# Kernel optimization log

Measured on AMD Instinct MI355X. Metric: run time of the kernel, lower is better.

Reference implementation:

```python
import jax, jax.numpy as jnp
import numpy as np

ALPHA = 0.2   # LeakyReLU slope
NEG = -9e15   # masked-attention fill, as in standard dense GAT


def _gat_multihead(h, edge_attr, adj, n2n, Wg, Weg, a_s, a_d, a_e, concat):
    # h: [N, I], edge_attr: [E, I], adj: [N, N], n2n: [N*N, I]
    # Wg, Weg: [H, I, O]; a_s, a_d, a_e: [H, O]
    H, I, O = Wg.shape
    N = h.shape[0]
    Wh = jnp.einsum('ni,hio->hno', h, Wg)                    # [H, N, O]
    es = jnp.einsum('hno,ho->hn', Wh, a_s)                   # [H, N] source logits
    ed = jnp.einsum('hno,ho->hn', Wh, a_d)                   # [H, N] dest logits
    ve = jnp.einsum('hio,ho->hi', Weg, a_e)                  # [H, I] fold edge proj into vector
    ee = (n2n @ ve.T).T.reshape(H, N, N)                     # [H, N, N] edge logits (row=src)
    e = jax.nn.leaky_relu(es[:, :, None] + ed[:, None, :] + ee, ALPHA)
    e = jnp.where(adj[None] > 0, e, NEG)
    attn = jax.nn.softmax(e, axis=-1)
    hout = jnp.einsum('hnm,hmo->nho', attn, Wh).reshape(N, H * O)
    eout = jnp.einsum('ei,hio->eho', edge_attr, Weg).reshape(-1, H * O)
    if concat:
        hout, eout = jax.nn.elu(hout), jax.nn.elu(eout)
    return hout, eout


def _edge_pool(x, edge_index, edge_attr, Wp, bp):
    # Deterministic static-shape variant of EdgePooling: merge node pairs (2k, 2k+1)
    # with a learned sigmoid score over the concatenated endpoint features.
    N, F = x.shape
    x2 = x.reshape(N // 2, 2, F)
    score = jax.nn.sigmoid(jnp.concatenate([x2[:, 0], x2[:, 1]], axis=1) @ Wp + bp)  # [N/2,1]
    new_x = (x2[:, 0] + x2[:, 1]) * score
    return new_x, edge_index // 2, edge_attr


def _global_attn(x, W, b):
    # GlobalAttention with gate_nn = Linear -> Sigmoid, softmax over the single graph
    gate = jax.nn.sigmoid(x @ W + b)          # [N, 1]
    alpha = jax.nn.softmax(gate, axis=0)
    return (alpha * x).sum(axis=0, keepdims=True)  # [1, F]


def _adj_n2n(N, edge_index, edge_attr):
    # Faithful vectorized version of _get_adj_node2node (scatter replaces python loop)
    src, dst = edge_index[0], edge_index[1]
    adj = jnp.zeros((N, N), edge_attr.dtype).at[src, dst].add(1.0)
    n2n = jnp.zeros((N * N, edge_attr.shape[1]), edge_attr.dtype).at[src * N + dst].set(edge_attr)
    return adj, n2n


def setup_inputs() -> dict:
    key = jax.random.key(0)
    ks = jax.random.split(key, 24)
    N, E, HID, NH = 512, 4096, 64, 16
    O = 2 * HID                                  # per-head GAT output = 128
    CAT = NH * O                                 # 2048
    s = 0.1
    features = jax.random.normal(ks[0], (N, HID), jnp.float32)
    edge_index = jax.random.randint(ks[1], (2, E), 0, N, jnp.int64)
    edge_attr = jax.random.normal(ks[2], (E, HID), jnp.float32)
    adjacency, n2n = _adj_n2n(N, edge_index, edge_attr)
    inp = dict(features=features, edge_index=edge_index, edge_attr=edge_attr,
               adjacency=adjacency, n2n=n2n)
    # SingleNodeAttentionLayer params
    inp['W_sn'] = jax.random.normal(ks[3], (HID, HID), jnp.float32) * s
    inp['a_sn'] = jax.random.normal(ks[4], (HID,), jnp.float32) * s
    # 16-head GAT layer (stacked over heads)
    inp['Wg'] = jax.random.normal(ks[5], (NH, HID, O), jnp.float32) * s
    inp['Weg'] = jax.random.normal(ks[6], (NH, HID, O), jnp.float32) * s
    inp['a_src'] = jax.random.normal(ks[7], (NH, O), jnp.float32) * s
    inp['a_dst'] = jax.random.normal(ks[8], (NH, O), jnp.float32) * s
    inp['a_edge'] = jax.random.normal(ks[9], (NH, O), jnp.float32) * s
    # edge_pool1 (in = NH*O = 2048)
    inp['Wp1'] = jax.random.normal(ks[10], (2 * CAT, 1), jnp.float32) * s
    inp['bp1'] = jnp.zeros((1,), jnp.float32)
    # out_att single head: 2048 -> 128
    inp['Wo'] = jax.random.normal(ks[11], (CAT, O), jnp.float32) * s
    inp['Weo'] = jax.random.normal(ks[12], (CAT, O), jnp.float32) * s
    inp['ao_src'] = jax.random.normal(ks[13], (O,), jnp.float32) * s
    inp['ao_dst'] = jax.random.normal(ks[14], (O,), jnp.float32) * s
    inp['ao_edge'] = jax.random.normal(ks[15], (O,), jnp.float32) * s
    # edge_pool2 (in = O = 128)
    inp['Wp2'] = jax.random.normal(ks[16], (2 * O, 1), jnp.float32) * s
    inp['bp2'] = jnp.zeros((1,), jnp.float32)
    # global-attention gates
    inp['g1W'] = jax.random.normal(ks[17], (HID, 1), jnp.float32) * s
    inp['g1b'] = jnp.zeros((1,), jnp.float32)
    inp['g2W'] = jax.random.normal(ks[18], (CAT, 1), jnp.float32) * s
    inp['g2b'] = jnp.zeros((1,), jnp.float32)
    inp['g3W'] = jax.random.normal(ks[19], (O, 1), jnp.float32) * s
    inp['g3b'] = jnp.zeros((1,), jnp.float32)
    return inp


def reference(features, edge_index, edge_attr, adjacency, n2n,
              W_sn, a_sn, Wg, Weg, a_src, a_dst, a_edge, Wp1, bp1,
              Wo, Weo, ao_src, ao_dst, ao_edge, Wp2, bp2,
              g1W, g1b, g2W, g2b, g3W, g3b):
    # SingleNodeAttentionLayer: per-node gated projection
    Wh0 = features @ W_sn
    coef = jax.nn.sigmoid(jax.nn.leaky_relu(Wh0 @ a_sn, ALPHA))
    h = jax.nn.elu(coef[:, None] * Wh0)                       # [N, HID]
    hs = [_global_attn(h, g1W, g1b)]
    # 16-head GAT (dropout inactive: training=False)
    h, ea = _gat_multihead(h, edge_attr, adjacency, n2n, Wg, Weg, a_src, a_dst, a_edge, True)
    h, ei, ea = _edge_pool(h, edge_index, ea, Wp1, bp1)
    hs.append(_global_attn(h, g2W, g2b))
    # rebuild dense adjacency + node2node features (scatter)
    adj2, n2n2 = _adj_n2n(h.shape[0], ei, ea)
    h, ea = _gat_multihead(h, ea, adj2, n2n2, Wo[None], Weo[None],
                           ao_src[None], ao_dst[None], ao_edge[None], False)
    h, ei, ea = _edge_pool(h, ei, ea, Wp2, bp2)
    hs.append(_global_attn(h, g3W, g3b))
    return jnp.concatenate(hs, axis=1)                        # [1, 64+2048+128]
```

## Files before the change

kernel.cpp:

```cpp
#include <hip/hip_runtime.h>
#include <hip/hip_bf16.h>

__device__ __forceinline__ float sigm(float x) { return 1.f / (1.f + expf(-x)); }
__device__ __forceinline__ float lrelu(float x) { return x > 0.f ? x : 0.2f * x; }
__device__ __forceinline__ float eluf(float x) { return x > 0.f ? x : expf(x) - 1.f; }

#define NEGF (-9e15f)
#define MAXD 40

__device__ __forceinline__ float wave_sum(float v) {
    #pragma unroll
    for (int off = 32; off >= 1; off >>= 1) v += __shfl_xor(v, off);
    return v;
}
__device__ __forceinline__ float wave_max(float v) {
    #pragma unroll
    for (int off = 32; off >= 1; off >>= 1) v = fmaxf(v, __shfl_xor(v, off));
    return v;
}
__device__ __forceinline__ float half_sum(float v) {
    #pragma unroll
    for (int off = 16; off >= 1; off >>= 1) v += __shfl_xor(v, off);
    return v;
}
__device__ __forceinline__ float half_max(float v) {
    #pragma unroll
    for (int off = 16; off >= 1; off >>= 1) v = fmaxf(v, __shfl_xor(v, off));
    return v;
}

__global__ void k_setup(const float* __restrict__ Wg, const float* __restrict__ Weg,
                        const float* __restrict__ asrc, const float* __restrict__ adst,
                        const float* __restrict__ aedge, const float* __restrict__ Weo,
                        const float* __restrict__ aoe,
                        const float* __restrict__ feat, const float* __restrict__ Wsn,
                        const float* __restrict__ asn, const float* __restrict__ g1W,
                        const float* __restrict__ g1b,
                        float* __restrict__ vs1, float* __restrict__ vd1, float* __restrict__ ve1,
                        float* __restrict__ ve2, int* __restrict__ winner,
                        float* __restrict__ h, float* __restrict__ gate1) {
    int b = blockIdx.x, t = threadIdx.x, w = t >> 6, l = t & 63;
    __shared__ float fr[4][64];
    if (b < 16) {
        int hd = b;
        float s0 = asrc[hd * 128 + l],  s1 = asrc[hd * 128 + 64 + l];
        float d0 = adst[hd * 128 + l],  d1 = adst[hd * 128 + 64 + l];
        float e0 = aedge[hd * 128 + l], e1 = aedge[hd * 128 + 64 + l];
        for (int i = w; i < 64; i += 4) {
            const float* Wr = Wg  + ((size_t)hd * 64 + i) * 128;
            const float* Er = Weg + ((size_t)hd * 64 + i) * 128;
            float w1 = Wr[l], w2 = Wr[64 + l];
            float q1 = Er[l], q2 = Er[64 + l];
            float pS = wave_sum(w1 * s0 + w2 * s1);
            float pD = wave_sum(w1 * d0 + w2 * d1);
            float pE = wave_sum(q1 * e0 + q2 * e1);
            if (l == 0) { vs1[hd * 64 + i] = pS; vd1[hd * 64 + i] = pD; ve1[hd * 64 + i] = pE; }
        }
    } else if (b < 32) {
        int base = (b - 16) * 128;
        float a0 = aoe[l], a1 = aoe[64 + l];
        for (int k = 0; k < 32; k++) {
            int c = base + w * 32 + k;
            const float* Wr = Weo + (size_t)c * 128;
            float p = wave_sum(Wr[l] * a0 + Wr[64 + l] * a1);
            if (l == 0) ve2[c] = p;
        }
    } else if (b < 48) {
        int base = (b - 32) * 4096;
        #pragma unroll
        for (int k = 0; k < 16; k++) winner[base + k * 256 + t] = -1;
    } else {
        int n = (b - 48) * 4 + w;
        fr[w][l] = feat[n * 64 + l];
        __syncthreads();
        float acc = 0.f;
        #pragma unroll 8
        for (int i = 0; i < 64; i++) acc += fr[w][i] * Wsn[i * 64 + l];
        float p = wave_sum(acc * asn[l]);
        float coef = sigm(lrelu(p));
        float hv = eluf(coef * acc);
        h[n * 64 + l] = hv;
        float g = wave_sum(hv * g1W[l]);
        if (l == 0) gate1[n] = sigm(g + g1b[0]);
    }
}

__global__ void k_mid(const float* __restrict__ h, const float* __restrict__ gate,
                      const float* __restrict__ vs1, const float* __restrict__ vd1,
                      const int* __restrict__ ei,
                      float* __restrict__ part1, float* __restrict__ es1, float* __restrict__ ed1,
                      int* __restrict__ winner) {
    int b = blockIdx.x, t = threadIdx.x;
    if (b < 8) {
        int nb = b, w = t >> 6, l = t & 63;
        __shared__ float mx[8], sm[8], al[512], pt[8][64];
        float g = gate[t];
        float m = wave_max(g);
        if (l == 0) mx[w] = m;
        __syncthreads();
        m = mx[0];
        #pragma unroll
        for (int i = 1; i < 8; i++) m = fmaxf(m, mx[i]);
        float p = expf(g - m);
        float Z = wave_sum(p);
        if (l == 0) sm[w] = Z;
        __syncthreads();
        Z = 0.f;
        #pragma unroll
        for (int i = 0; i < 8; i++) Z += sm[i];
        al[t] = p / Z;
        __syncthreads();
        int r0 = nb * 64 + w * 8;
        float acc = 0.f;
        #pragma unroll
        for (int r = 0; r < 8; r++) acc += al[r0 + r] * h[(r0 + r) * 64 + l];
        pt[w][l] = acc;
        __syncthreads();
        if (t < 64) {
            float o = 0.f;
            #pragma unroll
            for (int q = 0; q < 8; q++) o += pt[q][t];
            part1[nb * 64 + t] = o;
        }
    } else if (b < 24) {
        __shared__ float vsT[64][17], vdT[64][17];
        for (int idx = t; idx < 1024; idx += 512) {
            int i = idx & 63, hd = idx >> 6;
            vsT[i][hd] = vs1[hd * 64 + i];
            vdT[i][hd] = vd1[hd * 64 + i];
        }
        __syncthreads();
        int idx = (b - 8) * 512 + t;
        int n = idx >> 4, hd = idx & 15;
        const float* hr = h + n * 64;
        float aS = 0.f, aD = 0.f;
        #pragma unroll 8
        for (int i = 0; i < 64; i++) {
            float hv = hr[i];
            aS += hv * vsT[i][hd];
            aD += hv * vdT[i][hd];
        }
        es1[hd * 512 + n] = aS;
        ed1[hd * 512 + n] = aD;
    } else {
        int e = (b - 24) * 512 + t;
        int s = ei[e] >> 1, d = ei[4096 + e] >> 1;
        atomicMax(&winner[s * 256 + d], e);
    }
}

__global__ void k_attn_ze(const float* __restrict__ adj, const float* __restrict__ n2n,
                          const float* __restrict__ h, const float* __restrict__ ve1,
                          const float* __restrict__ es1, const float* __restrict__ ed1,
                          const float* __restrict__ eattr, const float* __restrict__ Weg,
                          const float* __restrict__ ve2,
                          float* __restrict__ z, float* __restrict__ d2) {
    int b = blockIdx.x, t = threadIdx.x, w = t >> 6, l = t & 63;
    if (b >= 512) {
        int e0 = (b - 512) * 8;
        int hd = t >> 5, q = t & 31;
        __shared__ float ea[8][64];
        __shared__ float sd2[8][8];
        ea[t >> 6][t & 63] = eattr[(size_t)(e0 + (t >> 6)) * 64 + (t & 63)];
        __syncthreads();
        float4 acc[8];
        #pragma unroll
        for (int r = 0; r < 8; r++) acc[r] = make_float4(0.f, 0.f, 0.f, 0.f);
        const float4* W4 = (const float4*)Weg + (size_t)hd * 2048 + q;
        #pragma unroll 4
        for (int i = 0; i < 64; i++) {
            float4 wv = W4[i * 32];
            #pragma unroll
            for (int r = 0; r < 8; r++) {
                float a = ea[r][i];
                acc[r].x += a * wv.x; acc[r].y += a * wv.y;
                acc[r].z += a * wv.z; acc[r].w += a * wv.w;
            }
        }
        float4 v2 = ((const float4*)ve2)[hd * 32 + q];
        #pragma unroll
        for (int r = 0; r < 8; r++) {
            float p = eluf(acc[r].x) * v2.x + eluf(acc[r].y) * v2.y
                    + eluf(acc[r].z) * v2.z + eluf(acc[r].w) * v2.w;
            p = wave_sum(p);
            if (l == 0) sd2[r][w] = p;
        }
        __syncthreads();
        if (t < 8) {
            float s8 = 0.f;
            #pragma unroll
            for (int k = 0; k < 8; k++) s8 += sd2[t][k];
            d2[e0 + t] = s8;
        }
        return;
    }
    int s = b;
    __shared__ float vlT[64][17];
    __shared__ float hrow[MAXD][65], nrow[MAXD][65];
    __shared__ float eh[16][48], ah[16][48];
    __shared__ float esr[16];
    __shared__ int dlist[MAXD];
    __shared__ int wbase[8];
    __shared__ int nnz_s;
    __shared__ float part[8][64];

    for (int idx = t; idx < 1024; idx += 512) vlT[idx & 63][idx >> 6] = ve1[(idx >> 6) * 64 + (idx & 63)];
    if (t < 16) esr[t] = es1[t * 512 + s];
    float a = adj[s * 512 + t];
    unsigned long long mask = __ballot(a > 0.f);
    if (l == 0) wbase[w] = __popcll(mask);
    __syncthreads();
    if (t == 0) {
        int run = 0;
        #pragma unroll
        for (int i = 0; i < 8; i++) { int c = wbase[i]; wbase[i] = run; run += c; }
        nnz_s = run;
    }
    __syncthreads();
    if (a > 0.f) {
        int slot = wbase[w] + __popcll(mask & ((1ULL << l) - 1ULL));
        if (slot < MAXD) dlist[slot] = t;
    }
    __syncthreads();
    int nnz = min(nnz_s, MAXD);

    if (nnz == 0) {
        int i = t & 63, q = t >> 6;
        float acc = 0.f;
        for (int d = q * 64; d < q * 64 + 64; d++) acc += h[d * 64 + i];
        part[q][i] = acc;
        __syncthreads();
        if (t < 64) {
            float sum = 0.f;
            #pragma unroll
            for (int q2 = 0; q2 < 8; q2++) sum += part[q2][t];
            float v = sum * (1.f / 512.f);
            for (int hd = 0; hd < 16; hd++) z[(size_t)s * 1024 + hd * 64 + t] = v;
        }
        return;
    }

    for (int base = 0; base < nnz; base += 8) {
        int j = base + (t >> 6);
        if (j < nnz) {
            int d = dlist[j];
            hrow[j][l] = h[d * 64 + l];
            nrow[j][l] = n2n[((size_t)s * 512 + d) * 64 + l];
        }
    }
    __syncthreads();
    for (int jb = 0; jb < nnz; jb += 32) {
        int j = jb + (t >> 4), hd = t & 15;
        if (j < nnz) {
            float ee = 0.f;
            #pragma unroll 8
            for (int i = 0; i < 64; i++) ee += nrow[j][i] * vlT[i][hd];
            eh[hd][j] = lrelu(esr[hd] + ed1[hd * 512 + dlist[j]] + ee);
        }
    }
    __syncthreads();
    {
        int hd = t >> 5, lane32 = t & 31;
        float v0 = (lane32 < nnz) ? eh[hd][lane32] : -1e30f;
        float v1 = (lane32 + 32 < nnz) ? eh[hd][lane32 + 32] : -1e30f;
        float m = half_max(fmaxf(v0, v1));
        float p0 = (lane32 < nnz) ? expf(v0 - m) : 0.f;
        float p1 = (lane32 + 32 < nnz) ? expf(v1 - m) : 0.f;
        float Z = half_sum(p0 + p1);
        float inv = 1.f / Z;
        if (lane32 < nnz) ah[hd][lane32] = p0 * inv;
        if (lane32 + 32 < nnz) ah[hd][lane32 + 32] = p1 * inv;
    }
    __syncthreads();
    int hd = t >> 5, i0 = t & 31;
    float a0 = 0.f, a1 = 0.f;
    for (int j = 0; j < nnz; j++) {
        float aj = ah[hd][j];
        a0 += aj * hrow[j][i0];
        a1 += aj * hrow[j][i0 + 32];
    }
    z[(size_t)s * 1024 + hd * 64 + i0]      = a0;
    z[(size_t)s * 1024 + hd * 64 + i0 + 32] = a1;
}

__global__ void k_big2p(const float* __restrict__ z, const float* __restrict__ Wg,
                        const float* __restrict__ Wp1, const float* __restrict__ bp1,
                        const float* __restrict__ g2W, const float* __restrict__ g2b,
                        const float* __restrict__ Wo,
                        const float* __restrict__ aos, const float* __restrict__ aod,
                        float* __restrict__ x1p, float* __restrict__ gate2,
                        float* __restrict__ Wh2, float* __restrict__ es2, float* __restrict__ ed2) {
    int b = blockIdx.x, t = threadIdx.x;
    __shared__ __align__(16) char smem[57600];
    float (*zt)[1024]    = reinterpret_cast<float(*)[1024]>(smem);
    float (*xr)[2048]    = reinterpret_cast<float(*)[2048]>(smem);
    float (*hs)[2048]    = reinterpret_cast<float(*)[2048]>(smem + 16384);
    float (*part)[2][128]= reinterpret_cast<float(*)[2][128]>(smem + 49152);
    float *red = reinterpret_cast<float*>(smem + 57344);
    float *rs  = reinterpret_cast<float*>(smem + 57408);
    float *rd  = reinterpret_cast<float*>(smem + 57424);
    int n0 = 2 * b;
    for (int idx = t; idx < 4096; idx += 1024)
        zt[idx >> 10][idx & 1023] = z[(size_t)(4 * b) * 1024 + idx];
    __syncthreads();
    {
        int c = t & 127, g8 = t >> 7;
        #pragma unroll
        for (int it = 0; it < 2; it++) {
            int hd = g8 + 8 * it;
            const float* W = Wg + (size_t)hd * 8192 + c;
            const float* z0 = &zt[0][hd * 64];
            const float* z1 = &zt[1][hd * 64];
            const float* z2 = &zt[2][hd * 64];
            const float* z3 = &zt[3][hd * 64];
            float a0 = 0.f, a1 = 0.f, a2 = 0.f, a3 = 0.f;
            #pragma unroll 8
            for (int i = 0; i < 64; i++) {
                float wv = W[(size_t)i * 128];
                a0 += z0[i] * wv; a1 += z1[i] * wv;
                a2 += z2[i] * wv; a3 += z3[i] * wv;
            }
            hs[0][hd * 128 + c] = eluf(a0);
            hs[1][hd * 128 + c] = eluf(a1);
            hs[2][hd * 128 + c] = eluf(a2);
            hs[3][hd * 128 + c] = eluf(a3);
        }
    }
    __syncthreads();
    int g = t >> 9, tt = t & 511;
    float p = 0.f;
    for (int f = tt; f < 2048; f += 512)
        p += hs[2 * g][f] * Wp1[f] + hs[2 * g + 1][f] * Wp1[2048 + f];
    p = wave_sum(p);
    if ((t & 63) == 0) red[t >> 6] = p;
    __syncthreads();
    float s8 = 0.f;
    #pragma unroll
    for (int k2 = 0; k2 < 8; k2++) s8 += red[g * 8 + k2];
    float sc = sigm(s8 + bp1[0]);
    __syncthreads();
    float pg = 0.f;
    for (int f = tt; f < 2048; f += 512) {
        float v = (hs[2 * g][f] + hs[2 * g + 1][f]) * sc;
        xr[g][f] = v;
        x1p[(size_t)(n0 + g) * 2048 + f] = v;
        pg += v * g2W[f];
    }
    pg = wave_sum(pg);
    if ((t & 63) == 0) red[t >> 6] = pg;
    __syncthreads();
    if (t == 0 || t == 512) {
        float sg8 = 0.f;
        #pragma unroll
        for (int k2 = 0; k2 < 8; k2++) sg8 += red[g * 8 + k2];
        gate2[n0 + g] = sigm(sg8 + g2b[0]);
    }
    int ks = t >> 7, c = t & 127;
    float a0 = 0.f, a1 = 0.f;
    const float* W  = Wo + (size_t)(ks * 256) * 128 + c;
    const float* x0 = xr[0] + ks * 256;
    const float* x1 = xr[1] + ks * 256;
    #pragma unroll 8
    for (int i = 0; i < 256; i++) { float w = W[(size_t)i * 128]; a0 += x0[i] * w; a1 += x1[i] * w; }
    part[ks][0][c] = a0;
    part[ks][1][c] = a1;
    __syncthreads();
    if (t < 256) {
        int r = t >> 7, cc = t & 127;
        float a = 0.f;
        #pragma unroll
        for (int k2 = 0; k2 < 8; k2++) a += part[k2][r][cc];
        Wh2[(n0 + r) * 128 + cc] = a;
        float ps = wave_sum(a * aos[cc]);
        float pd = wave_sum(a * aod[cc]);
        if ((t & 63) == 0) { rs[t >> 6] = ps; rd[t >> 6] = pd; }
    }
    __syncthreads();
    if (t == 0) { es2[n0] = rs[0] + rs[1]; ed2[n0] = rd[0] + rd[1]; }
    if (t == 1) { es2[n0 + 1] = rs[2] + rs[3]; ed2[n0 + 1] = rd[2] + rd[3]; }
}

__global__ void k_fin(const int* __restrict__ winner, const float* __restrict__ d2,
                      const float* __restrict__ es2, const float* __restrict__ ed2,
                      const float* __restrict__ Wh2, const float* __restrict__ gate2,
                      const float* __restrict__ x1p,
                      float* __restrict__ part2, float* __restrict__ hout2) {
    int b = blockIdx.x, t = threadIdx.x;
    if (b < 256) {
        int s = b, w = t >> 6, l = t & 63;
        __shared__ float mx[4], sm[4], at[256], part[2][128];
        int win = winner[s * 256 + t];
        float e;
        if (win >= 0) e = lrelu(es2[s] + ed2[t] + d2[win]);
        else e = NEGF;
        float m = wave_max(e);
        if (l == 0) mx[w] = m;
        __syncthreads();
        m = fmaxf(fmaxf(mx[0], mx[1]), fmaxf(mx[2], mx[3]));
        float p = expf(e - m);
        float Z = wave_sum(p);
        if (l == 0) sm[w] = Z;
        __syncthreads();
        Z = sm[0] + sm[1] + sm[2] + sm[3];
        at[t] = p / Z;
        __syncthreads();
        int c = t & 127, hf = t >> 7;
        float acc = 0.f;
        for (int d = hf * 128; d < hf * 128 + 128; d++)
            acc += at[d] * Wh2[d * 128 + c];
        part[hf][c] = acc;
        __syncthreads();
        if (t < 128) hout2[s * 128 + t] = part[0][t] + part[1][t];
    } else {
        int tile = b - 256;
        int cb = tile >> 3, nb = tile & 7;
        __shared__ float mx2[4], sm2[4], al[256];
        int w = t >> 6, l = t & 63;
        float g = gate2[t];
        float m = wave_max(g);
        if (l == 0) mx2[w] = m;
        __syncthreads();
        m = fmaxf(fmaxf(mx2[0], mx2[1]), fmaxf(mx2[2], mx2[3]));
        float p = expf(g - m);
        float Z = wave_sum(p);
        if (l == 0) sm2[w] = Z;
        __syncthreads();
        Z = sm2[0] + sm2[1] + sm2[2] + sm2[3];
        al[t] = p / Z;
        __syncthreads();
        int c = cb * 256 + t;
        int n0 = nb * 32;
        float acc = 0.f;
        #pragma unroll 8
        for (int n = n0; n < n0 + 32; n++) acc += al[n] * x1p[(size_t)n * 2048 + c];
        part2[nb * 2048 + c] = acc;
    }
}

__global__ void k_tail(const float* __restrict__ hout2, const float* __restrict__ Wp,
                       const float* __restrict__ bp, const float* __restrict__ g3W,
                       const float* __restrict__ g3b, const float* __restrict__ part1,
                       const float* __restrict__ part2, float* __restrict__ out) {
    int t = threadIdx.x, w = t >> 6, l = t & 63;
    if (blockIdx.x > 0) {
        int rb = blockIdx.x - 1;
        if (rb == 0) {
            if (t < 64) {
                float o = 0.f;
                #pragma unroll
                for (int nb = 0; nb < 8; nb++) o += part1[nb * 64 + t];
                out[t] = o;
            }
        } else if (t < 256) {
            int c = (rb - 1) * 256 + t;
            float o = 0.f;
            #pragma unroll
            for (int nb = 0; nb < 8; nb++) o += part2[nb * 2048 + c];
            out[64 + c] = o;
        }
        return;
    }
    __shared__ float x2s[128][129];
    __shared__ float gt[128];
    __shared__ float mx[2], sm[2], al[128], part[4][128];
    float bpv = bp[0], g3bv = g3b[0];
    for (int rr = 0; rr < 16; rr++) {
        int k = w * 16 + rr;
        float a0  = hout2[(size_t)(2 * k) * 128 + l];
        float a0b = hout2[(size_t)(2 * k) * 128 + 64 + l];
        float a1  = hout2[(size_t)(2 * k + 1) * 128 + l];
        float a1b = hout2[(size_t)(2 * k + 1) * 128 + 64 + l];
        float p = a0 * Wp[l] + a0b * Wp[64 + l] + a1 * Wp[128 + l] + a1b * Wp[192 + l];
        p = wave_sum(p);
        float sc = sigm(p + bpv);
        float v  = (a0 + a1) * sc;
        float vb = (a0b + a1b) * sc;
        x2s[k][l] = v;
        x2s[k][64 + l] = vb;
        float g = wave_sum(v * g3W[l] + vb * g3W[64 + l]);
        if (l == 0) gt[k] = sigm(g + g3bv);
    }
    __syncthreads();
    if (t < 128) {
        float g = gt[t];
        float m = wave_max(g);
        if (l == 0) mx[w] = m;
    }
    __syncthreads();
    if (t < 128) {
        float g = gt[t];
        float m = fmaxf(mx[0], mx[1]);
        float p = expf(g - m);
        float Z = wave_sum(p);
        if (l == 0) sm[w] = Z;
        al[t] = p;
    }
    __syncthreads();
    float invZ = 1.f / (sm[0] + sm[1]);
    int q = t >> 7, c = t & 127;
    float acc = 0.f;
    for (int n = q * 32; n < q * 32 + 32; n++) acc += al[n] * x2s[n][c];
    part[q][c] = acc * invZ;
    __syncthreads();
    if (t < 128) out[2112 + t] = part[0][t] + part[1][t] + part[2][t] + part[3][t];
}

extern "C" void kernel_launch(void* const* d_in, const int* in_sizes, int n_in,
                              void* d_out, int out_size, void* d_ws, size_t ws_size,
                              hipStream_t stream) {
    const float* feat  = (const float*)d_in[0];
    const int*   eidx  = (const int*)d_in[1];
    const float* eattr = (const float*)d_in[2];
    const float* adj   = (const float*)d_in[3];
    const float* n2n   = (const float*)d_in[4];
    const float* Wsn   = (const float*)d_in[5];
    const float* asn   = (const float*)d_in[6];
    const float* Wg    = (const float*)d_in[7];
    const float* Weg   = (const float*)d_in[8];
    const float* asrc  = (const float*)d_in[9];
    const float* adst  = (const float*)d_in[10];
    const float* aedge = (const float*)d_in[11];
    const float* Wp1   = (const float*)d_in[12];
    const float* bp1   = (const float*)d_in[13];
    const float* Wo    = (const float*)d_in[14];
    const float* Weo   = (const float*)d_in[15];
    const float* aos   = (const float*)d_in[16];
    const float* aod   = (const float*)d_in[17];
    const float* aoe   = (const float*)d_in[18];
    const float* Wp2   = (const float*)d_in[19];
    const float* bp2   = (const float*)d_in[20];
    const float* g1W   = (const float*)d_in[21];
    const float* g1b   = (const float*)d_in[22];
    const float* g2W   = (const float*)d_in[23];
    const float* g2b   = (const float*)d_in[24];
    const float* g3W   = (const float*)d_in[25];
    const float* g3b   = (const float*)d_in[26];
    float* out = (float*)d_out;

    char* ws = (char*)d_ws;
    float* h      = (float*)(ws + 0x0000000);
    float* z      = (float*)(ws + 0x0020000);
    float* ve1    = (float*)(ws + 0x0430000);
    float* ve2    = (float*)(ws + 0x0431000);
    float* gate1  = (float*)(ws + 0x0433000);
    float* gate2  = (float*)(ws + 0x0434000);
    float* vs1    = (float*)(ws + 0x0436000);
    float* vd1    = (float*)(ws + 0x0438000);
    float* es1    = (float*)(ws + 0x0440000);
    float* ed1    = (float*)(ws + 0x0448000);
    float* d2     = (float*)(ws + 0x1840000);
    float* x1p    = (float*)(ws + 0x1850000);
    int*   winner = (int*)  (ws + 0x1A50000);
    float* Wh2    = (float*)(ws + 0x1A90000);
    float* es2    = (float*)(ws + 0x1AB0000);
    float* ed2    = (float*)(ws + 0x1AB1000);
    float* hout2  = (float*)(ws + 0x1AB2000);
    float* part2  = (float*)(ws + 0x1AE2000);
    float* part1  = (float*)(ws + 0x1AF2000);

    k_setup  <<<176, 256, 0, stream>>>(Wg, Weg, asrc, adst, aedge, Weo, aoe,
                                       feat, Wsn, asn, g1W, g1b,
                                       vs1, vd1, ve1, ve2, winner, h, gate1);
    k_mid    <<<32, 512, 0, stream>>>(h, gate1, vs1, vd1, eidx, part1, es1, ed1, winner);
    k_attn_ze<<<1024, 512, 0, stream>>>(adj, n2n, h, ve1, es1, ed1, eattr, Weg, ve2, z, d2);
    k_big2p  <<<128, 1024, 0, stream>>>(z, Wg, Wp1, bp1, g2W, g2b, Wo, aos, aod,
                                        x1p, gate2, Wh2, es2, ed2);
    k_fin    <<<320, 256, 0, stream>>>(winner, d2, es2, ed2, Wh2, gate2, x1p, part2, hout2);
    k_tail   <<<10, 512, 0, stream>>>(hout2, Wp2, bp2, g3W, g3b, part1, part2, out);
}
```

Before: 121.4 us.

## Fold k_mid into k_attn_ze and compute source/dest logits on the fly

New measurement: 116.9 us, median of 2. 3.7% less time.

```diff
diff --git a/kernel.cpp b/kernel.cpp
--- a/kernel.cpp
+++ b/kernel.cpp
@@ -85,16 +85,25 @@
     }
 }
 
-__global__ void k_mid(const float* __restrict__ h, const float* __restrict__ gate,
-                      const float* __restrict__ vs1, const float* __restrict__ vd1,
-                      const int* __restrict__ ei,
-                      float* __restrict__ part1, float* __restrict__ es1, float* __restrict__ ed1,
-                      int* __restrict__ winner) {
-    int b = blockIdx.x, t = threadIdx.x;
-    if (b < 8) {
-        int nb = b, w = t >> 6, l = t & 63;
+__global__ void k_attn_ze(const float* __restrict__ adj, const float* __restrict__ n2n,
+                          const float* __restrict__ h, const float* __restrict__ ve1,
+                          const float* __restrict__ vs1, const float* __restrict__ vd1,
+                          const float* __restrict__ eattr, const float* __restrict__ Weg,
+                          const float* __restrict__ ve2, const float* __restrict__ gate1,
+                          const int* __restrict__ ei,
+                          float* __restrict__ z, float* __restrict__ d2,
+                          float* __restrict__ part1, int* __restrict__ winner) {
+    int b = blockIdx.x, t = threadIdx.x, w = t >> 6, l = t & 63;
+    if (b >= 1032) {
+        int e = (b - 1032) * 512 + t;
+        int s = ei[e] >> 1, d = ei[4096 + e] >> 1;
+        atomicMax(&winner[s * 256 + d], e);
+        return;
+    }
+    if (b >= 1024) {
+        int nb = b - 1024;
         __shared__ float mx[8], sm[8], al[512], pt[8][64];
-        float g = gate[t];
+        float g = gate1[t];
         float m = wave_max(g);
         if (l == 0) mx[w] = m;
         __syncthreads();
@@ -122,40 +131,8 @@
             for (int q = 0; q < 8; q++) o += pt[q][t];
             part1[nb * 64 + t] = o;
         }
-    } else if (b < 24) {
-        __shared__ float vsT[64][17], vdT[64][17];
-        for (int idx = t; idx < 1024; idx += 512) {
-            int i = idx & 63, hd = idx >> 6;
-            vsT[i][hd] = vs1[hd * 64 + i];
-            vdT[i][hd] = vd1[hd * 64 + i];
-        }
-        __syncthreads();
-        int idx = (b - 8) * 512 + t;
-        int n = idx >> 4, hd = idx & 15;
-        const float* hr = h + n * 64;
-        float aS = 0.f, aD = 0.f;
-        #pragma unroll 8
-        for (int i = 0; i < 64; i++) {
-            float hv = hr[i];
-            aS += hv * vsT[i][hd];
-            aD += hv * vdT[i][hd];
-        }
-        es1[hd * 512 + n] = aS;
-        ed1[hd * 512 + n] = aD;
-    } else {
-        int e = (b - 24) * 512 + t;
-        int s = ei[e] >> 1, d = ei[4096 + e] >> 1;
-        atomicMax(&winner[s * 256 + d], e);
-    }
-}
-
-__global__ void k_attn_ze(const float* __restrict__ adj, const float* __restrict__ n2n,
-                          const float* __restrict__ h, const float* __restrict__ ve1,
-                          const float* __restrict__ es1, const float* __restrict__ ed1,
-                          const float* __restrict__ eattr, const float* __restrict__ Weg,
-                          const float* __restrict__ ve2,
-                          float* __restrict__ z, float* __restrict__ d2) {
-    int b = blockIdx.x, t = threadIdx.x, w = t >> 6, l = t & 63;
+        return;
+    }
     if (b >= 512) {
         int e0 = (b - 512) * 8;
         int hd = t >> 5, q = t & 31;
@@ -195,17 +172,23 @@
         return;
     }
     int s = b;
-    __shared__ float vlT[64][17];
+    __shared__ float vlT[64][17], vsT[64][17], vdT[64][17];
+    __shared__ float hsr[64];
     __shared__ float hrow[MAXD][65], nrow[MAXD][65];
     __shared__ float eh[16][48], ah[16][48];
-    __shared__ float esr[16];
+    __shared__ float es_s[16];
     __shared__ int dlist[MAXD];
     __shared__ int wbase[8];
     __shared__ int nnz_s;
     __shared__ float part[8][64];
 
-    for (int idx = t; idx < 1024; idx += 512) vlT[idx & 63][idx >> 6] = ve1[(idx >> 6) * 64 + (idx & 63)];
-    if (t < 16) esr[t] = es1[t * 512 + s];
+    for (int idx = t; idx < 1024; idx += 512) {
+        int i = idx & 63, hd = idx >> 6;
+        vlT[i][hd] = ve1[hd * 64 + i];
+        vsT[i][hd] = vs1[hd * 64 + i];
+        vdT[i][hd] = vd1[hd * 64 + i];
+    }
+    if (t < 64) hsr[t] = h[s * 64 + t];
     float a = adj[s * 512 + t];
     unsigned long long mask = __ballot(a > 0.f);
     if (l == 0) wbase[w] = __popcll(mask);
@@ -248,14 +231,22 @@
             nrow[j][l] = n2n[((size_t)s * 512 + d) * 64 + l];
         }
     }
+    if (t < 16) {
+        float acc = 0.f;
+        for (int i = 0; i < 64; i++) acc += hsr[i] * vsT[i][t];
+        es_s[t] = acc;
+    }
     __syncthreads();
     for (int jb = 0; jb < nnz; jb += 32) {
         int j = jb + (t >> 4), hd = t & 15;
         if (j < nnz) {
-            float ee = 0.f;
+            float ee = 0.f, edv = 0.f;
             #pragma unroll 8
-            for (int i = 0; i < 64; i++) ee += nrow[j][i] * vlT[i][hd];
-            eh[hd][j] = lrelu(esr[hd] + ed1[hd * 512 + dlist[j]] + ee);
+            for (int i = 0; i < 64; i++) {
+                ee  += nrow[j][i] * vlT[i][hd];
+                edv += hrow[j][i] * vdT[i][hd];
+            }
+            eh[hd][j] = lrelu(es_s[hd] + edv + ee);
         }
     }
     __syncthreads();
@@ -546,8 +537,6 @@
     float* gate2  = (float*)(ws + 0x0434000);
     float* vs1    = (float*)(ws + 0x0436000);
     float* vd1    = (float*)(ws + 0x0438000);
-    float* es1    = (float*)(ws + 0x0440000);
-    float* ed1    = (float*)(ws + 0x0448000);
     float* d2     = (float*)(ws + 0x1840000);
     float* x1p    = (float*)(ws + 0x1850000);
     int*   winner = (int*)  (ws + 0x1A50000);
@@ -561,8 +550,8 @@
     k_setup  <<<176, 256, 0, stream>>>(Wg, Weg, asrc, adst, aedge, Weo, aoe,
                                        feat, Wsn, asn, g1W, g1b,
                                        vs1, vd1, ve1, ve2, winner, h, gate1);
-    k_mid    <<<32, 512, 0, stream>>>(h, gate1, vs1, vd1, eidx, part1, es1, ed1, winner);
-    k_attn_ze<<<1024, 512, 0, stream>>>(adj, n2n, h, ve1, es1, ed1, eattr, Weg, ve2, z, d2);
+    k_attn_ze<<<1040, 512, 0, stream>>>(adj, n2n, h, ve1, vs1, vd1, eattr, Weg, ve2,
+                                        gate1, eidx, z, d2, part1, winner);
     k_big2p  <<<128, 1024, 0, stream>>>(z, Wg, Wp1, bp1, g2W, g2b, Wo, aos, aod,
                                         x1p, gate2, Wh2, es2, ed2);
     k_fin    <<<320, 256, 0, stream>>>(winner, d2, es2, ed2, Wh2, gate2, x1p, part2, hout2);
```
